# Kernel tuning notes

Hardware: AMD Instinct MI355X
Metric: run time of the kernel (lower is better)

Reference implementation:

```python
import jax, jax.numpy as jnp
import numpy as np

D = 1024

def setup_inputs() -> dict:
    key = jax.random.key(0)
    ks = jax.random.split(key, 7)
    s = 1.0 / np.sqrt(D)
    x = jax.random.normal(ks[0], (4, 4096, D), dtype=jnp.float32)
    Wq = jax.random.uniform(ks[1], (D, D), jnp.float32, -s, s)
    bq = jax.random.uniform(ks[2], (D,), jnp.float32, -s, s)
    Wk = jax.random.uniform(ks[3], (D, D), jnp.float32, -s, s)
    bk = jax.random.uniform(ks[4], (D,), jnp.float32, -s, s)
    Wv = jax.random.uniform(ks[5], (D, D), jnp.float32, -s, s)
    bv = jax.random.uniform(ks[6], (D,), jnp.float32, -s, s)
    return {"x": x, "Wq": Wq, "bq": bq, "Wk": Wk, "bk": bk, "Wv": Wv, "bv": bv}

def reference(x, Wq, bq, Wk, bk, Wv, bv):
    # nn.Linear: y = x @ W.T + b
    q = (jnp.einsum('bnd,ed->bne', x, Wq) + bq) / jnp.sqrt(jnp.float32(Wq.shape[0]))
    k = jnp.einsum('bnd,ed->bne', x, Wk) + bk
    v = jnp.einsum('bnd,ed->bne', x, Wv) + bv
    scores = jnp.einsum('bqd,bkd->bqk', q, k)  # [B,N,N]
    N = scores.shape[-1]
    mask = jnp.triu(jnp.full((N, N), -1e9, dtype=scores.dtype), k=1)
    probs = jax.nn.softmax(scores + mask, axis=-1)
    return jnp.einsum('bqk,bkd->bqd', probs, v)
```

## Files before the change

kernel.cpp:

```cpp
#include <hip/hip_runtime.h>
#include <hip/hip_bf16.h>
#include <stdint.h>


typedef __attribute__((ext_vector_type(8))) short short8;
typedef __attribute__((ext_vector_type(4))) float float4v;

__device__ inline unsigned short f2b(float f) {
  union { float f; unsigned u; } v; v.f = f;
  unsigned r = (v.u + 0x7fffu + ((v.u >> 16) & 1u)) >> 16;
  return (unsigned short)r;
}
__device__ inline float b2f(unsigned short b) {
  union { unsigned u; float f; } v; v.u = ((unsigned)b) << 16;
  return v.f;
}

typedef const __attribute__((address_space(1))) unsigned int* gptr_t;
typedef __attribute__((address_space(3))) unsigned int* lptr_t;

__device__ inline void gload_lds16(const unsigned short* g, unsigned short* l) {
  __builtin_amdgcn_global_load_lds((gptr_t)(const void*)g, (lptr_t)(void*)l, 16, 0, 0);
}

__global__ __launch_bounds__(256) void cvt_all(const float* __restrict__ x,
                                               const float* __restrict__ wq,
                                               const float* __restrict__ wk,
                                               const float* __restrict__ wv,
                                               unsigned short* __restrict__ xb,
                                               unsigned short* __restrict__ wb) {
  const float* src;
  unsigned short* dst;
  long n, i0, stride;
  if (blockIdx.x < 2048) {
    src = x; dst = xb; n = 16384L * 1024;
    i0 = ((long)blockIdx.x * 256 + threadIdx.x) * 4;
    stride = 2048L * 256 * 4;
  } else {
    int wsec = (blockIdx.x - 2048) >> 8;
    int blk = (blockIdx.x - 2048) & 255;
    src = wsec == 0 ? wq : (wsec == 1 ? wk : wv);
    dst = wb + (long)wsec * 1024 * 1024;
    n = 1024L * 1024;
    i0 = ((long)blk * 256 + threadIdx.x) * 4;
    stride = 256L * 256 * 4;
  }
  for (long i = i0; i < n; i += stride) {
    float4 f = *(const float4*)&src[i];
    union { unsigned short u[4]; uint2 v; } o;
    o.u[0] = f2b(f.x); o.u[1] = f2b(f.y); o.u[2] = f2b(f.z); o.u[3] = f2b(f.w);
    *(uint2*)&dst[i] = o.v;
  }
}


__device__ __forceinline__ void stage_half(const unsigned short* __restrict__ g,
                                           int grow0, int tile, int kk,
                                           char* tb, int tid) {
  const int kc = tile * 64 + kk * 32;
#pragma unroll
  for (int j = 0; j < 2; j++) {
    int c = j * 512 + tid;
    int lc = c ^ ((c >> 3) & 3);
    gload_lds16(g + (long)(grow0 + (lc >> 2)) * 1024 + kc + (lc & 3) * 8,
                (unsigned short*)(tb + kk * 16384 + (j * 512 + (tid & 448)) * 16));
  }
}

#define DSA(dst, TB, kk, mi) do { \
  int o = (kk) * 16384 + (wr * 128 + (mi) * 16 + lr) * 64 + g16; \
  o ^= ((o >> 3) & 0x30); dst = *(const short8*)((TB) + o); } while (0)
#define DSB(dst, TB, kk, ni) do { \
  int o = (kk) * 16384 + (wc * 64 + (ni) * 16 + lr) * 64 + g16; \
  o ^= ((o >> 3) & 0x30); dst = *(const short8*)((TB) + o); } while (0)

#define MF(x, y, z) __builtin_amdgcn_mfma_f32_16x16x32_bf16(x, y, z, 0, 0, 0)
#define MMQ(M0) \
  acc[M0 + 0][0] = MF(a0, b0, acc[M0 + 0][0]); \
  acc[M0 + 0][1] = MF(a0, b1, acc[M0 + 0][1]); \
  acc[M0 + 0][2] = MF(a0, b2, acc[M0 + 0][2]); \
  acc[M0 + 0][3] = MF(a0, b3, acc[M0 + 0][3]); \
  acc[M0 + 1][0] = MF(a1, b0, acc[M0 + 1][0]); \
  acc[M0 + 1][1] = MF(a1, b1, acc[M0 + 1][1]); \
  acc[M0 + 1][2] = MF(a1, b2, acc[M0 + 1][2]); \
  acc[M0 + 1][3] = MF(a1, b3, acc[M0 + 1][3]); \
  acc[M0 + 2][0] = MF(a2, b0, acc[M0 + 2][0]); \
  acc[M0 + 2][1] = MF(a2, b1, acc[M0 + 2][1]); \
  acc[M0 + 2][2] = MF(a2, b2, acc[M0 + 2][2]); \
  acc[M0 + 2][3] = MF(a2, b3, acc[M0 + 2][3]); \
  acc[M0 + 3][0] = MF(a3, b0, acc[M0 + 3][0]); \
  acc[M0 + 3][1] = MF(a3, b1, acc[M0 + 3][1]); \
  acc[M0 + 3][2] = MF(a3, b2, acc[M0 + 3][2]); \
  acc[M0 + 3][3] = MF(a3, b3, acc[M0 + 3][3]);

#define KTILE(AT, BT, OA, t) do { \
  short8 a0, a1, a2, a3, b0, b1, b2, b3; \
   \
  DSB(b0, BT, 0, 0); DSB(b1, BT, 0, 1); DSB(b2, BT, 0, 2); DSB(b3, BT, 0, 3); \
  DSA(a0, AT, 0, 0); DSA(a1, AT, 0, 1); DSA(a2, AT, 0, 2); DSA(a3, AT, 0, 3); \
  if ((t) + 1 < NT) stage_half(A, rowA0, (t) + 1, 1, OA, tid); \
  __builtin_amdgcn_s_barrier(); \
  __builtin_amdgcn_s_setprio(1); MMQ(0); __builtin_amdgcn_s_setprio(0); \
  __builtin_amdgcn_s_barrier(); \
   \
  DSA(a0, AT, 0, 4); DSA(a1, AT, 0, 5); DSA(a2, AT, 0, 6); DSA(a3, AT, 0, 7); \
  if ((t) + 2 < NT) stage_half(Bm, rowB0, (t) + 2, 0, BT, tid); \
  __builtin_amdgcn_s_barrier(); \
  __builtin_amdgcn_s_setprio(1); MMQ(4); __builtin_amdgcn_s_setprio(0); \
  __builtin_amdgcn_s_barrier(); \
   \
  DSB(b0, BT, 1, 0); DSB(b1, BT, 1, 1); DSB(b2, BT, 1, 2); DSB(b3, BT, 1, 3); \
  DSA(a0, AT, 1, 0); DSA(a1, AT, 1, 1); DSA(a2, AT, 1, 2); DSA(a3, AT, 1, 3); \
  if ((t) + 2 < NT) stage_half(A, rowA0, (t) + 2, 0, AT, tid); \
  __builtin_amdgcn_s_barrier(); \
  __builtin_amdgcn_s_setprio(1); MMQ(0); __builtin_amdgcn_s_setprio(0); \
  __builtin_amdgcn_s_barrier(); \
   \
  DSA(a0, AT, 1, 4); DSA(a1, AT, 1, 5); DSA(a2, AT, 1, 6); DSA(a3, AT, 1, 7); \
  if ((t) + 2 < NT) stage_half(Bm, rowB0, (t) + 2, 1, BT, tid); \
  __builtin_amdgcn_s_barrier(); \
  __builtin_amdgcn_s_setprio(1); MMQ(4); __builtin_amdgcn_s_setprio(0); \
  if ((t) + 2 < NT) { asm volatile("s_waitcnt vmcnt(6)" ::: "memory"); } \
  else               { asm volatile("s_waitcnt vmcnt(0)" ::: "memory"); } \
  __builtin_amdgcn_s_barrier(); \
} while (0)

template <int MODE>
__global__ __launch_bounds__(512, 2) void gemm8p(
    const unsigned short* __restrict__ Ag, const unsigned short* __restrict__ Bg,
    const float* __restrict__ b0v, const float* __restrict__ b1v,
    const float* __restrict__ b2v, void* __restrict__ Cg,
    long sA, long sB, long sC) {
  __shared__ __align__(16) char smem[131072];
  const int NT = 16;

  int bi, bj, b;
  if (MODE == 0) {
    bi = blockIdx.x; bj = blockIdx.y; b = 0;
  } else {
    int t = blockIdx.x % 136;
    b = blockIdx.x / 136;
    int r = (int)((sqrtf(8.0f * t + 1.0f) - 1.0f) * 0.5f);
    while ((r + 1) * (r + 2) / 2 <= t) r++;
    while (r * (r + 1) / 2 > t) r--;
    bi = r; bj = t - r * (r + 1) / 2;
  }

  const unsigned short* A = Ag + (long)b * sA;
  const unsigned short* Bm = Bg + (long)b * sB;

  const int tid = threadIdx.x;
  const int l = tid & 63, w = tid >> 6;
  const int wr = w >> 2, wc = w & 3;
  const int lr = l & 15, g16 = (l >> 4) * 16;
  const int rowA0 = bi * 256, rowB0 = bj * 256;

  char* A0 = smem;
  char* B0 = smem + 32768;
  char* A1 = smem + 65536;
  char* B1 = smem + 98304;

  float4v acc[8][4];
#pragma unroll
  for (int i = 0; i < 8; i++)
#pragma unroll
    for (int j = 0; j < 4; j++) acc[i][j] = (float4v){0.f, 0.f, 0.f, 0.f};

  stage_half(A, rowA0, 0, 0, A0, tid);
  stage_half(Bm, rowB0, 0, 0, B0, tid);
  stage_half(A, rowA0, 0, 1, A0, tid);
  stage_half(Bm, rowB0, 0, 1, B0, tid);
  stage_half(Bm, rowB0, 1, 0, B1, tid);
  stage_half(A, rowA0, 1, 0, A1, tid);
  stage_half(Bm, rowB0, 1, 1, B1, tid);
  asm volatile("s_waitcnt vmcnt(6)" ::: "memory");
  __builtin_amdgcn_s_barrier();

#pragma unroll 1
  for (int t = 0; t < NT; t += 2) {
    KTILE(A0, B0, A1, t);
    KTILE(A1, B1, A0, t + 1);
  }

  if (MODE == 0) {
    const int sec = bj >> 2;
    const float* bias = sec == 0 ? b0v : (sec == 1 ? b1v : b2v);
    const float scale = sec == 0 ? 0.03125f : 1.0f;
    unsigned short* C = (unsigned short*)Cg + (long)sec * 16777216L;
    const int colbase = (bj & 3) * 256 + wc * 64;
#pragma unroll
    for (int mi = 0; mi < 8; mi++) {
      int rbase = bi * 256 + wr * 128 + mi * 16 + (l >> 4) * 4;
#pragma unroll
      for (int ni = 0; ni < 4; ni++) {
        int col = colbase + ni * 16 + lr;
        float bb = bias[col];
#pragma unroll
        for (int j = 0; j < 4; j++)
          C[(long)(rbase + j) * 1024 + col] = f2b((acc[mi][ni][j] + bb) * scale);
      }
    }
  } else {
    unsigned short* C = (unsigned short*)Cg + (long)b * sC;
#pragma unroll
    for (int mi = 0; mi < 8; mi++) {
      int rbase = bi * 256 + wr * 128 + mi * 16 + (l >> 4) * 4;
#pragma unroll
      for (int ni = 0; ni < 4; ni++) {
        int col = bj * 256 + wc * 64 + ni * 16 + lr;
#pragma unroll
        for (int j = 0; j < 4; j++)
          C[(long)(rbase + j) * 4096 + col] = f2b(acc[mi][ni][j]);
      }
    }
  }
}

__global__ __launch_bounds__(256) void gemm_pv(const unsigned short* __restrict__ Ag,
                                               const unsigned short* __restrict__ Bg,
                                               float* __restrict__ Cg,
                                               int N, int K,
                                               long sA, long sB, long sC) {
  const int b = blockIdx.z;
  const unsigned short* A = Ag + (long)b * sA;
  const unsigned short* B = Bg + (long)b * sB;
  const int bj = blockIdx.y;
  int biArr[2] = {(int)blockIdx.x, 31 - (int)blockIdx.x};

  __shared__ unsigned short As[128 * 32];
  __shared__ unsigned short Bs[128 * 32];

  const int tid = threadIdx.x;
  const int w = tid >> 6, l = tid & 63;
  const int wr = w >> 1, wc = w & 1;
  const int lr = l & 15;
  const int k8 = (l >> 4) * 8;
  const int rowB0 = bj * 128;

#pragma unroll
  for (int tt = 0; tt < 2; tt++) {
    const int bi = biArr[tt];
    const int rowA0 = bi * 128;
    int cap = (bi + 1) * 128;
    int Keff = cap < K ? cap : K;

    float4v acc[4][4];
#pragma unroll
    for (int i = 0; i < 4; i++)
#pragma unroll
      for (int j = 0; j < 4; j++) acc[i][j] = (float4v){0.f, 0.f, 0.f, 0.f};

    for (int k0 = 0; k0 < Keff; k0 += 32) {
#pragma unroll
      for (int i = 0; i < 2; i++) {
        int c = i * 256 + tid;
        int r = c >> 2, c8 = (c & 3) * 8;
        int ldsbase = (i * 256 + w * 64) * 8;
        gload_lds16(A + (long)(rowA0 + r) * K + k0 + c8, &As[ldsbase]);
        gload_lds16(B + (long)(rowB0 + r) * K + k0 + c8, &Bs[ldsbase]);
      }
      __syncthreads();

      short8 af[4], bf[4];
#pragma unroll
      for (int mi = 0; mi < 4; mi++)
        af[mi] = *(const short8*)&As[(wr * 64 + mi * 16 + lr) * 32 + k8];
#pragma unroll
      for (int ni = 0; ni < 4; ni++)
        bf[ni] = *(const short8*)&Bs[(wc * 64 + ni * 16 + lr) * 32 + k8];
#pragma unroll
      for (int mi = 0; mi < 4; mi++)
#pragma unroll
        for (int ni = 0; ni < 4; ni++)
          acc[mi][ni] = __builtin_amdgcn_mfma_f32_16x16x32_bf16(af[mi], bf[ni], acc[mi][ni], 0, 0, 0);
      __syncthreads();
    }

    float* C = Cg + (long)b * sC;
    const int col0 = bj * 128 + wc * 64;
    const int row0g = bi * 128 + wr * 64;
#pragma unroll
    for (int mi = 0; mi < 4; mi++) {
      int rbase = row0g + mi * 16 + (l >> 4) * 4;
#pragma unroll
      for (int ni = 0; ni < 4; ni++) {
        int col = col0 + ni * 16 + lr;
#pragma unroll
        for (int j = 0; j < 4; j++)
          C[(long)(rbase + j) * N + col] = acc[mi][ni][j];
      }
    }
  }
}

__global__ __launch_bounds__(256) void softmax_causal(unsigned short* __restrict__ S) {
  const int bid = blockIdx.x;
  const int b = bid >> 12, i = bid & 4095;
  unsigned short* row = S + ((long)b * 4096 + i) * 4096;
  const int len = i + 1;
  const int padTo = ((i >> 7) + 1) << 7;
  const int nch = padTo >> 3;
  const int tid = threadIdx.x;
  const int w = tid >> 6;

  float v[2][8];
  int nc[2];
  float m = -3e38f;
#pragma unroll
  for (int s = 0; s < 2; s++) {
    int c = tid + s * 256;
    nc[s] = -1;
    if (c < nch) {
      nc[s] = c;
      short8 x = *(const short8*)&row[c * 8];
#pragma unroll
      for (int j = 0; j < 8; j++) {
        int idx = c * 8 + j;
        float f = (idx < len) ? b2f((unsigned short)x[j]) : -3e38f;
        v[s][j] = f;
        m = fmaxf(m, f);
      }
    }
  }

  __shared__ float red[4];
#pragma unroll
  for (int off = 32; off; off >>= 1) m = fmaxf(m, __shfl_xor(m, off));
  if ((tid & 63) == 0) red[w] = m;
  __syncthreads();
  m = fmaxf(fmaxf(red[0], red[1]), fmaxf(red[2], red[3]));

  float sum = 0.f;
#pragma unroll
  for (int s = 0; s < 2; s++) {
    if (nc[s] >= 0) {
#pragma unroll
      for (int j = 0; j < 8; j++) {
        float e = __expf(v[s][j] - m);
        v[s][j] = e;
        sum += e;
      }
    }
  }
  __syncthreads();
#pragma unroll
  for (int off = 32; off; off >>= 1) sum += __shfl_xor(sum, off);
  if ((tid & 63) == 0) red[w] = sum;
  __syncthreads();
  sum = red[0] + red[1] + red[2] + red[3];
  const float inv = 1.0f / sum;

#pragma unroll
  for (int s = 0; s < 2; s++) {
    if (nc[s] >= 0) {
      int c = nc[s];
      short8 o;
#pragma unroll
      for (int j = 0; j < 8; j++) o[j] = (short)f2b(v[s][j] * inv);
      *(short8*)&row[c * 8] = o;
    }
  }
}

__global__ __launch_bounds__(256) void transpose_v(const unsigned short* __restrict__ V,
                                                   unsigned short* __restrict__ VT) {
  __shared__ unsigned short t[64][65];
  const int b = blockIdx.z;
  const int n0 = blockIdx.x * 64;
  const int d0 = blockIdx.y * 64;
  const unsigned short* Vb = V + (long)b * 4096 * 1024;
  unsigned short* VTb = VT + (long)b * 1024 * 4096;
  const int tid = threadIdx.x;
#pragma unroll
  for (int s = 0; s < 2; s++) {
    int c = s * 256 + tid;
    int r = c >> 3, c8 = (c & 7) * 8;
    short8 x = *(const short8*)&Vb[(long)(n0 + r) * 1024 + d0 + c8];
#pragma unroll
    for (int j = 0; j < 8; j++) t[r][c8 + j] = (unsigned short)x[j];
  }
  __syncthreads();
#pragma unroll
  for (int s = 0; s < 2; s++) {
    int c = s * 256 + tid;
    int dr = c >> 3, n8 = (c & 7) * 8;
    short8 o;
#pragma unroll
    for (int j = 0; j < 8; j++) o[j] = (short)t[n8 + j][dr];
    *(short8*)&VTb[(long)(d0 + dr) * 4096 + n0 + n8] = o;
  }
}

extern "C" void kernel_launch(void* const* d_in, const int* in_sizes, int n_in,
                              void* d_out, int out_size, void* d_ws, size_t ws_size,
                              hipStream_t stream) {
  const float* x  = (const float*)d_in[0];
  const float* Wq = (const float*)d_in[1];
  const float* bq = (const float*)d_in[2];
  const float* Wk = (const float*)d_in[3];
  const float* bk = (const float*)d_in[4];
  const float* Wv = (const float*)d_in[5];
  const float* bv = (const float*)d_in[6];
  float* out = (float*)d_out;

  const long NTOK = 16384L;
  const long D = 1024L;
  const long NB = 4096L;

  unsigned short* ws = (unsigned short*)d_ws;
  unsigned short* qb = ws;
  unsigned short* kb = qb + NTOK * D;
  unsigned short* vb = kb + NTOK * D;
  unsigned short* vT = vb + NTOK * D;
  unsigned short* S  = vT + NTOK * D;
  unsigned short* xb  = S;
  unsigned short* Wb  = S + NTOK * D;

  cvt_all<<<2048 + 3 * 256, 256, 0, stream>>>(x, Wq, Wk, Wv, xb, Wb);

  gemm8p<0><<<dim3(64, 12), 512, 0, stream>>>(xb, Wb, bq, bk, bv, qb, 0, 0, 0);

  transpose_v<<<dim3(64, 16, 4), 256, 0, stream>>>(vb, vT);

  gemm8p<1><<<544, 512, 0, stream>>>(qb, kb, nullptr, nullptr, nullptr, S,
      NB * D, NB * D, NB * NB);

  softmax_causal<<<16384, 256, 0, stream>>>(S);

  gemm_pv<<<dim3(16, 8, 4), 256, 0, stream>>>(S, vT, out,
      1024, 4096, NB * NB, D * NB, NB * D);
}
```

Baseline: 493.9 us.

## Replace PV GEMM with pipelined 256x128 tile kernel pairing causal row blocks

The simple double-sync PV GEMM is replaced with a 512-thread kernel using 256-row tiles and 64-wide K steps. It uses double-buffered swizzled LDS staged via global_load_lds, with barrier-split MFMA phases and setprio, like the QK kernel. Each block processes a light and a heavy causal row block (bi and 15-bi) in one continuous pipeline, so every block does the same 68 K-tiles. Softmax padding is raised to 256 columns to match the larger causal tile. The cost is more zero work in the padded region and fewer blocks (256) for the grid.

```diff
diff --git a/kernel.cpp b/kernel.cpp
--- a/kernel.cpp
+++ b/kernel.cpp
@@ -53,7 +53,6 @@
   }
 }
 
-
 __device__ __forceinline__ void stage_half(const unsigned short* __restrict__ g,
                                            int grow0, int tile, int kk,
                                            char* tb, int tid) {
@@ -95,27 +94,23 @@
 
 #define KTILE(AT, BT, OA, t) do { \
   short8 a0, a1, a2, a3, b0, b1, b2, b3; \
-   \
   DSB(b0, BT, 0, 0); DSB(b1, BT, 0, 1); DSB(b2, BT, 0, 2); DSB(b3, BT, 0, 3); \
   DSA(a0, AT, 0, 0); DSA(a1, AT, 0, 1); DSA(a2, AT, 0, 2); DSA(a3, AT, 0, 3); \
   if ((t) + 1 < NT) stage_half(A, rowA0, (t) + 1, 1, OA, tid); \
   __builtin_amdgcn_s_barrier(); \
   __builtin_amdgcn_s_setprio(1); MMQ(0); __builtin_amdgcn_s_setprio(0); \
   __builtin_amdgcn_s_barrier(); \
-   \
   DSA(a0, AT, 0, 4); DSA(a1, AT, 0, 5); DSA(a2, AT, 0, 6); DSA(a3, AT, 0, 7); \
   if ((t) + 2 < NT) stage_half(Bm, rowB0, (t) + 2, 0, BT, tid); \
   __builtin_amdgcn_s_barrier(); \
   __builtin_amdgcn_s_setprio(1); MMQ(4); __builtin_amdgcn_s_setprio(0); \
   __builtin_amdgcn_s_barrier(); \
-   \
   DSB(b0, BT, 1, 0); DSB(b1, BT, 1, 1); DSB(b2, BT, 1, 2); DSB(b3, BT, 1, 3); \
   DSA(a0, AT, 1, 0); DSA(a1, AT, 1, 1); DSA(a2, AT, 1, 2); DSA(a3, AT, 1, 3); \
   if ((t) + 2 < NT) stage_half(A, rowA0, (t) + 2, 0, AT, tid); \
   __builtin_amdgcn_s_barrier(); \
   __builtin_amdgcn_s_setprio(1); MMQ(0); __builtin_amdgcn_s_setprio(0); \
   __builtin_amdgcn_s_barrier(); \
-   \
   DSA(a0, AT, 1, 4); DSA(a1, AT, 1, 5); DSA(a2, AT, 1, 6); DSA(a3, AT, 1, 7); \
   if ((t) + 2 < NT) stage_half(Bm, rowB0, (t) + 2, 1, BT, tid); \
   __builtin_amdgcn_s_barrier(); \
@@ -216,81 +211,143 @@
   }
 }
 
-__global__ __launch_bounds__(256) void gemm_pv(const unsigned short* __restrict__ Ag,
-                                               const unsigned short* __restrict__ Bg,
-                                               float* __restrict__ Cg,
-                                               int N, int K,
-                                               long sA, long sB, long sC) {
+
+__device__ __forceinline__ void pv_src(int tt, int NT1, int bi, int bi2,
+                                       int* ar, int* kc) {
+  if (tt < NT1) { *ar = bi << 8; *kc = tt << 6; }
+  else          { *ar = bi2 << 8; *kc = (tt - NT1) << 6; }
+}
+
+__device__ __forceinline__ void pv_stageA(const unsigned short* __restrict__ g,
+                                          int ar, int kc, int kk, char* tb, int tid) {
+#pragma unroll
+  for (int j = 0; j < 2; j++) {
+    int c = j * 512 + tid;
+    int lc = c ^ ((c >> 3) & 3);
+    gload_lds16(g + (long)(ar + (lc >> 2)) * 4096 + kc + kk * 32 + (lc & 3) * 8,
+                (unsigned short*)(tb + kk * 16384 + (j * 512 + (tid & 448)) * 16));
+  }
+}
+
+__device__ __forceinline__ void pv_stageB(const unsigned short* __restrict__ g,
+                                          int br, int kc, char* tb, int tid) {
+#pragma unroll
+  for (int kk = 0; kk < 2; kk++) {
+    int lc = tid ^ ((tid >> 3) & 3);
+    gload_lds16(g + (long)(br + (lc >> 2)) * 4096 + kc + kk * 32 + (lc & 3) * 8,
+                (unsigned short*)(tb + kk * 8192 + (tid & 448) * 16));
+  }
+}
+
+#define PDSA(dst, TB, kk, mi) do { \
+  int o = (kk) * 16384 + (wr * 64 + (mi) * 16 + lr) * 64 + g16; \
+  o ^= ((o >> 3) & 0x30); dst = *(const short8*)((TB) + o); } while (0)
+#define PDSB(dst, TB, kk, ni) do { \
+  int o = (kk) * 8192 + (wc * 64 + (ni) * 16 + lr) * 64 + g16; \
+  o ^= ((o >> 3) & 0x30); dst = *(const short8*)((TB) + o); } while (0)
+
+#define PMM \
+  acc[0][0] = MF(a0, b0, acc[0][0]); acc[0][1] = MF(a0, b1, acc[0][1]); \
+  acc[0][2] = MF(a0, b2, acc[0][2]); acc[0][3] = MF(a0, b3, acc[0][3]); \
+  acc[1][0] = MF(a1, b0, acc[1][0]); acc[1][1] = MF(a1, b1, acc[1][1]); \
+  acc[1][2] = MF(a1, b2, acc[1][2]); acc[1][3] = MF(a1, b3, acc[1][3]); \
+  acc[2][0] = MF(a2, b0, acc[2][0]); acc[2][1] = MF(a2, b1, acc[2][1]); \
+  acc[2][2] = MF(a2, b2, acc[2][2]); acc[2][3] = MF(a2, b3, acc[2][3]); \
+  acc[3][0] = MF(a3, b0, acc[3][0]); acc[3][1] = MF(a3, b1, acc[3][1]); \
+  acc[3][2] = MF(a3, b2, acc[3][2]); acc[3][3] = MF(a3, b3, acc[3][3]);
+
+#define PVTILE(CA, CB, OA, OB, t) do { \
+  short8 a0, a1, a2, a3, b0, b1, b2, b3; \
+  PDSB(b0, CB, 0, 0); PDSB(b1, CB, 0, 1); PDSB(b2, CB, 0, 2); PDSB(b3, CB, 0, 3); \
+  PDSA(a0, CA, 0, 0); PDSA(a1, CA, 0, 1); PDSA(a2, CA, 0, 2); PDSA(a3, CA, 0, 3); \
+  if ((t) + 1 < 68) { \
+    int ar_, kc_; pv_src((t) + 1, NT1, bi, bi2, &ar_, &kc_); \
+    pv_stageA(Sb, ar_, kc_, 1, OA, tid); \
+    pv_stageB(vTb, brow0, kc_, OB, tid); \
+  } \
+  __builtin_amdgcn_s_barrier(); \
+  __builtin_amdgcn_s_setprio(1); PMM; __builtin_amdgcn_s_setprio(0); \
+  __builtin_amdgcn_s_barrier(); \
+  PDSB(b0, CB, 1, 0); PDSB(b1, CB, 1, 1); PDSB(b2, CB, 1, 2); PDSB(b3, CB, 1, 3); \
+  PDSA(a0, CA, 1, 0); PDSA(a1, CA, 1, 1); PDSA(a2, CA, 1, 2); PDSA(a3, CA, 1, 3); \
+  if ((t) + 2 < 68) { \
+    int ar_, kc_; pv_src((t) + 2, NT1, bi, bi2, &ar_, &kc_); \
+    pv_stageA(Sb, ar_, kc_, 0, CA, tid); \
+  } \
+  __builtin_amdgcn_s_barrier(); \
+  __builtin_amdgcn_s_setprio(1); PMM; __builtin_amdgcn_s_setprio(0); \
+  if ((t) + 2 < 68) { asm volatile("s_waitcnt vmcnt(2)" ::: "memory"); } \
+  else              { asm volatile("s_waitcnt vmcnt(0)" ::: "memory"); } \
+  __builtin_amdgcn_s_barrier(); \
+} while (0)
+
+#define PV_STORE(row0) do { \
+  float* C = Cg + (long)b * 4194304L; \
+  _Pragma("unroll") for (int mi = 0; mi < 4; mi++) { \
+    int rbase = (row0) + wr * 64 + mi * 16 + (l >> 4) * 4; \
+    _Pragma("unroll") for (int ni = 0; ni < 4; ni++) { \
+      int col = brow0 + wc * 64 + ni * 16 + lr; \
+      _Pragma("unroll") for (int j = 0; j < 4; j++) \
+        C[(long)(rbase + j) * 1024 + col] = acc[mi][ni][j]; \
+    } \
+  } \
+} while (0)
+
+__global__ __launch_bounds__(512, 2) void pv8p(const unsigned short* __restrict__ Sg,
+                                               const unsigned short* __restrict__ vTg,
+                                               float* __restrict__ Cg) {
+  __shared__ __align__(16) char smem[98304];
+  const int bi = blockIdx.x;
+  const int bj = blockIdx.y;
   const int b = blockIdx.z;
-  const unsigned short* A = Ag + (long)b * sA;
-  const unsigned short* B = Bg + (long)b * sB;
-  const int bj = blockIdx.y;
-  int biArr[2] = {(int)blockIdx.x, 31 - (int)blockIdx.x};
-
-  __shared__ unsigned short As[128 * 32];
-  __shared__ unsigned short Bs[128 * 32];
+  const int bi2 = 15 - bi;
+  const int NT1 = 4 * (bi + 1);
+
+  const unsigned short* Sb = Sg + (long)b * 16777216L;
+  const unsigned short* vTb = vTg + (long)b * 4194304L;
+  const int brow0 = bj * 128;
 
   const int tid = threadIdx.x;
-  const int w = tid >> 6, l = tid & 63;
+  const int l = tid & 63, w = tid >> 6;
   const int wr = w >> 1, wc = w & 1;
-  const int lr = l & 15;
-  const int k8 = (l >> 4) * 8;
-  const int rowB0 = bj * 128;
-
-#pragma unroll
-  for (int tt = 0; tt < 2; tt++) {
-    const int bi = biArr[tt];
-    const int rowA0 = bi * 128;
-    int cap = (bi + 1) * 128;
-    int Keff = cap < K ? cap : K;
-
-    float4v acc[4][4];
-#pragma unroll
-    for (int i = 0; i < 4; i++)
-#pragma unroll
-      for (int j = 0; j < 4; j++) acc[i][j] = (float4v){0.f, 0.f, 0.f, 0.f};
-
-    for (int k0 = 0; k0 < Keff; k0 += 32) {
-#pragma unroll
-      for (int i = 0; i < 2; i++) {
-        int c = i * 256 + tid;
-        int r = c >> 2, c8 = (c & 3) * 8;
-        int ldsbase = (i * 256 + w * 64) * 8;
-        gload_lds16(A + (long)(rowA0 + r) * K + k0 + c8, &As[ldsbase]);
-        gload_lds16(B + (long)(rowB0 + r) * K + k0 + c8, &Bs[ldsbase]);
-      }
-      __syncthreads();
-
-      short8 af[4], bf[4];
-#pragma unroll
-      for (int mi = 0; mi < 4; mi++)
-        af[mi] = *(const short8*)&As[(wr * 64 + mi * 16 + lr) * 32 + k8];
-#pragma unroll
-      for (int ni = 0; ni < 4; ni++)
-        bf[ni] = *(const short8*)&Bs[(wc * 64 + ni * 16 + lr) * 32 + k8];
-#pragma unroll
-      for (int mi = 0; mi < 4; mi++)
-#pragma unroll
-        for (int ni = 0; ni < 4; ni++)
-          acc[mi][ni] = __builtin_amdgcn_mfma_f32_16x16x32_bf16(af[mi], bf[ni], acc[mi][ni], 0, 0, 0);
-      __syncthreads();
-    }
-
-    float* C = Cg + (long)b * sC;
-    const int col0 = bj * 128 + wc * 64;
-    const int row0g = bi * 128 + wr * 64;
-#pragma unroll
-    for (int mi = 0; mi < 4; mi++) {
-      int rbase = row0g + mi * 16 + (l >> 4) * 4;
-#pragma unroll
-      for (int ni = 0; ni < 4; ni++) {
-        int col = col0 + ni * 16 + lr;
-#pragma unroll
-        for (int j = 0; j < 4; j++)
-          C[(long)(rbase + j) * N + col] = acc[mi][ni][j];
-      }
-    }
-  }
+  const int lr = l & 15, g16 = (l >> 4) * 16;
+
+  char* XA = smem;
+  char* YA = smem + 32768;
+  char* XB = smem + 65536;
+  char* YB = smem + 81920;
+
+  float4v acc[4][4];
+#pragma unroll
+  for (int i = 0; i < 4; i++)
+#pragma unroll
+    for (int j = 0; j < 4; j++) acc[i][j] = (float4v){0.f, 0.f, 0.f, 0.f};
+
+  {
+    int ar_, kc_;
+    pv_src(0, NT1, bi, bi2, &ar_, &kc_);
+    pv_stageA(Sb, ar_, kc_, 0, XA, tid);
+    pv_stageA(Sb, ar_, kc_, 1, XA, tid);
+    pv_stageB(vTb, brow0, kc_, XB, tid);
+    pv_src(1, NT1, bi, bi2, &ar_, &kc_);
+    pv_stageA(Sb, ar_, kc_, 0, YA, tid);
+  }
+  asm volatile("s_waitcnt vmcnt(2)" ::: "memory");
+  __builtin_amdgcn_s_barrier();
+
+#pragma unroll 1
+  for (int t = 0; t < 68; t += 2) {
+    if (t == NT1) {
+      PV_STORE(bi * 256);
+#pragma unroll
+      for (int i = 0; i < 4; i++)
+#pragma unroll
+        for (int j = 0; j < 4; j++) acc[i][j] = (float4v){0.f, 0.f, 0.f, 0.f};
+    }
+    PVTILE(XA, XB, YA, YB, t);
+    PVTILE(YA, YB, XA, XB, t + 1);
+  }
+  PV_STORE(bi2 * 256);
 }
 
 __global__ __launch_bounds__(256) void softmax_causal(unsigned short* __restrict__ S) {
@@ -298,7 +355,7 @@
   const int b = bid >> 12, i = bid & 4095;
   unsigned short* row = S + ((long)b * 4096 + i) * 4096;
   const int len = i + 1;
-  const int padTo = ((i >> 7) + 1) << 7;
+  const int padTo = ((i >> 8) + 1) << 8;
   const int nch = padTo >> 3;
   const int tid = threadIdx.x;
   const int w = tid >> 6;
@@ -427,6 +484,5 @@
 
   softmax_causal<<<16384, 256, 0, stream>>>(S);
 
-  gemm_pv<<<dim3(16, 8, 4), 256, 0, stream>>>(S, vT, out,
-      1024, 4096, NB * NB, D * NB, NB * D);
-}
+  pv8p<<<dim3(8, 8, 4), 512, 0, stream>>>(S, vT, out);
+}
```

Result: faster. 448.9 us (-9.1%).
